# Kernel optimization log

Hardware: AMD Instinct MI355X
Metric: run time of the kernel (lower is better)

## Reference

```python
import jax, jax.numpy as jnp
import numpy as np


def setup_inputs() -> dict:
    key = jax.random.key(0)
    ks = jax.random.split(key, 5)
    B, S, F = 32, 2048, 64
    s = lambda d: 1.0 / np.sqrt(d)
    return {
        "x": jax.random.normal(ks[0], (B, S, F), jnp.float32),
        "Wq": jax.random.normal(ks[1], (F, 24), jnp.float32) * s(F),
        "Wk": jax.random.normal(ks[2], (F, 24), jnp.float32) * s(F),
        "Wv": jax.random.normal(ks[3], (F, 32), jnp.float32) * s(F),
        "Wh": jax.random.normal(ks[4], (32, F), jnp.float32) * s(32),
    }


def reference(x, Wq, Wk, Wv, Wh):
    # x: [B, S, F]
    q = jnp.einsum("bsf,fd->bsd", x, Wq)  # [B, S, 24]
    k = jnp.einsum("bsf,fd->bsd", x, Wk)  # [B, S, 24]
    v = jnp.einsum("bsf,fd->bsd", x, Wv)  # [B, S, 32]
    a = jnp.einsum("bqd,bkd->bqk", q, k)  # [B, S, S]
    # NOTE: softmax over dim=1 (query axis), as in the original module
    a = jax.nn.softmax(a, axis=1)
    h1 = jnp.einsum("bqk,bkd->bqd", a, v)  # [B, S, 32]
    return jnp.einsum("bsd,df->bsf", h1, Wh)  # [B, S, F]
```

## Files before the change

kernel.cpp:

```cpp
#include <hip/hip_runtime.h>
#include <hip/hip_fp16.h>

#define SS 2048
#define L2E 1.44269504088896340736f

typedef _Float16 f16x4 __attribute__((ext_vector_type(4)));
typedef _Float16 f16x8 __attribute__((ext_vector_type(8)));
typedef float f32x4 __attribute__((ext_vector_type(4)));

#define GLDS16(g, l) __builtin_amdgcn_global_load_lds(                          \
    (const __attribute__((address_space(1))) void*)(g),                         \
    (__attribute__((address_space(3))) void*)(l), 16, 0, 0)
#define GLDS4(g, l) __builtin_amdgcn_global_load_lds(                           \
    (const __attribute__((address_space(1))) void*)(g),                         \
    (__attribute__((address_space(3))) void*)(l), 4, 0, 0)

__global__ __launch_bounds__(256) void qkv_kernel(
    const float* __restrict__ x, const float* __restrict__ Wq,
    const float* __restrict__ Wk, const float* __restrict__ Wv,
    _Float16* __restrict__ qfp, _Float16* __restrict__ kfp,
    _Float16* __restrict__ vfp)
{
    __shared__ float xsT[64 * 64];
    __shared__ float wc[64 * 96];

    int t = threadIdx.x;
    for (int i = t; i < 384; i += 256) {
        float4 v = ((const float4*)Wq)[i];
        int f = (i * 4) / 24, c = (i * 4) % 24;
        *(float4*)&wc[f * 96 + c] = v;
    }
    for (int i = t; i < 384; i += 256) {
        float4 v = ((const float4*)Wk)[i];
        int f = (i * 4) / 24, c = (i * 4) % 24;
        *(float4*)&wc[f * 96 + 24 + c] = v;
    }
    for (int i = t; i < 512; i += 256) {
        float4 v = ((const float4*)Wv)[i];
        int f = i >> 3, c = (i * 4) & 31;
        *(float4*)&wc[f * 96 + 48 + c] = v;
    }
    {
        int f = t >> 2, seg = t & 3;
        *(float4*)&wc[f * 96 + 80 + seg * 4] = (float4){0.f, 0.f, 0.f, 0.f};
    }
    long rowbase = (long)blockIdx.x * 64;
    const float4* xg = (const float4*)(x + rowbase * 64);
    for (int i = t; i < 1024; i += 256) {
        int r = i >> 4, c4 = i & 15;
        float4 v = xg[i];
        xsT[(c4 * 4 + 0) * 64 + r] = v.x;
        xsT[(c4 * 4 + 1) * 64 + r] = v.y;
        xsT[(c4 * 4 + 2) * 64 + r] = v.z;
        xsT[(c4 * 4 + 3) * 64 + r] = v.w;
    }
    __syncthreads();

    int rg = t >> 3;
    int cg = t & 7;
    float acc0[12], acc1[12];
    #pragma unroll
    for (int i = 0; i < 12; ++i) acc0[i] = acc1[i] = 0.f;

    #pragma unroll 4
    for (int f = 0; f < 64; ++f) {
        float2 xv = *(const float2*)&xsT[f * 64 + rg * 2];
        const float* wr = &wc[f * 96 + cg * 12];
        float4 wA = *(const float4*)(wr);
        float4 wB = *(const float4*)(wr + 4);
        float4 wC = *(const float4*)(wr + 8);
        float wv_[12] = {wA.x, wA.y, wA.z, wA.w, wB.x, wB.y, wB.z, wB.w,
                         wC.x, wC.y, wC.z, wC.w};
        #pragma unroll
        for (int i = 0; i < 12; ++i) {
            acc0[i] += xv.x * wv_[i];
            acc1[i] += xv.y * wv_[i];
        }
    }
    __syncthreads();
    _Float16* os = (_Float16*)wc;

    if (t < 128) {
        int reg = t >> 6, rr = t & 63;
        *(f16x8*)&os[reg * 2048 + (rr >> 4) * 512 + (48 + (rr & 15)) * 8]
            = (f16x8){0, 0, 0, 0, 0, 0, 0, 0};
    }

    #pragma unroll
    for (int j = 0; j < 2; ++j) {
        int s = rg * 2 + j, st = s >> 4;
        const float* a = j ? acc1 : acc0;
        #pragma unroll
        for (int i = 0; i < 12; ++i) {
            int c = cg * 12 + i;
            if (c < 24) {
                os[st * 512 + ((c >> 3) * 16 + (s & 15)) * 8 + (c & 7)]
                    = (_Float16)(a[i] * L2E);
            } else if (c < 48) {
                int ck = c - 24;
                os[2048 + st * 512 + ((ck >> 3) * 16 + (s & 15)) * 8 + (ck & 7)]
                    = (_Float16)a[i];
            } else if (c < 80) {
                int vd = c - 48;
                os[4096 + st * 512 + (((s >> 2) & 3) * 16 + (vd & 15)) * 8
                   + (vd >> 4) * 4 + (s & 3)] = (_Float16)a[i];
            }
        }
    }
    __syncthreads();

    long blk = blockIdx.x;
    *(f16x8*)(qfp + blk * 2048 + t * 8) = *(const f16x8*)&os[t * 8];
    *(f16x8*)(kfp + blk * 2048 + t * 8) = *(const f16x8*)&os[2048 + t * 8];
    *(f16x8*)(vfp + blk * 2048 + t * 8) = *(const f16x8*)&os[4096 + t * 8];
}

__global__ __launch_bounds__(256) void stats_kernel(
    const _Float16* __restrict__ qf, const _Float16* __restrict__ kf,
    float* __restrict__ zpart)
{
    __shared__ __align__(16) _Float16 qtile[2][2048];
    int w = blockIdx.x;
    int b = w >> 6, rest = w & 63;
    int kb = rest >> 3, qs = rest & 7;
    int t = threadIdx.x;
    int wv = t >> 6, l = t & 63, llo = l & 15, lhi = l >> 4;

    const _Float16* kfb = kf + ((long)b * 128 + kb * 16 + wv * 4) * 512 + l * 8;
    f16x8 af[4];
    #pragma unroll
    for (int kt = 0; kt < 4; ++kt) af[kt] = *(const f16x8*)(kfb + kt * 512);

    const _Float16* qsrc = qf + ((long)b * 128 + qs * 16 + wv) * 512 + l * 8;
    f32x4 z[4] = {{0,0,0,0},{0,0,0,0},{0,0,0,0},{0,0,0,0}};

    GLDS16(qsrc, &qtile[0][wv * 512]);
    for (int rnd = 0; rnd < 4; ++rnd) {
        int cb = rnd & 1;
        __syncthreads();
        if (rnd < 3) GLDS16(qsrc + (rnd + 1) * 2048, &qtile[cb ^ 1][wv * 512]);
        #pragma unroll
        for (int fi = 0; fi < 4; ++fi) {
            f16x8 q0 = *(const f16x8*)&qtile[cb][fi * 512 + l * 8];
            #pragma unroll
            for (int kt = 0; kt < 4; ++kt) {
                f32x4 d = __builtin_amdgcn_mfma_f32_16x16x32_f16(af[kt], q0,
                            (f32x4){0.f, 0.f, 0.f, 0.f}, 0, 0, 0);
                #pragma unroll
                for (int r = 0; r < 4; ++r) z[kt][r] += __builtin_amdgcn_exp2f(d[r]);
            }
        }
    }
    #pragma unroll
    for (int m = 1; m < 16; m <<= 1)
        #pragma unroll
        for (int kt = 0; kt < 4; ++kt)
            #pragma unroll
            for (int r = 0; r < 4; ++r) z[kt][r] += __shfl_xor(z[kt][r], m, 64);
    if (llo == 0) {
        #pragma unroll
        for (int kt = 0; kt < 4; ++kt)
            *(f32x4*)(zpart + ((long)qs * 32 + b) * SS + kb * 256 + wv * 64
                      + kt * 16 + lhi * 4) = z[kt];
    }
}

__global__ __launch_bounds__(256) void finalize_kernel(
    const float* __restrict__ zpart, float* __restrict__ wneg)
{
    int i = blockIdx.x * 256 + threadIdx.x;
    float s = 0.f;
    #pragma unroll
    for (int qs = 0; qs < 8; ++qs) s += zpart[(long)qs * 32 * SS + i];
    wneg[i] = -__builtin_amdgcn_logf(s);
}

__global__ __launch_bounds__(256) void attn_out_kernel(
    const _Float16* __restrict__ qf, const _Float16* __restrict__ kf,
    const _Float16* __restrict__ vf, const float* __restrict__ wneg,
    const float* __restrict__ Wh, float* __restrict__ out)
{
    __shared__ __align__(16) _Float16 lds[2][4224];

    int w = blockIdx.x;
    int b = w >> 5, qblk = w & 31;
    int t = threadIdx.x;
    int wv = t >> 6, l = t & 63, llo = l & 15, lhi = l >> 4;
    int q0 = qblk * 64 + wv * 16;

    f16x8 qfr = *(const f16x8*)(qf + ((long)b * 128 + qblk * 4 + wv) * 512 + l * 8);

    f16x4 whlo[4], whhi[4];
    #pragma unroll
    for (int fb = 0; fb < 4; ++fb)
        #pragma unroll
        for (int j = 0; j < 4; ++j) {
            whlo[fb][j] = (_Float16)Wh[(4 * lhi + j) * 64 + fb * 16 + llo];
            whhi[fb][j] = (_Float16)Wh[(16 + 4 * lhi + j) * 64 + fb * 16 + llo];
        }

    const _Float16* kgb = kf + ((long)b * 128 + wv) * 512 + l * 8;
    const _Float16* vgb = vf + (long)b * 65536 + wv * 512 + l * 8;
    const float*    wgb = wneg + (long)b * SS + l;

    f32x4 acc0 = {0,0,0,0}, acc1 = {0,0,0,0};

    GLDS16(kgb, &lds[0][wv * 512]);
    GLDS16(vgb, &lds[0][2048 + wv * 512]);
    if (wv == 0) GLDS4(wgb, (float*)&lds[0][4096]);

    for (int tile = 0; tile < 32; ++tile) {
        int cb = tile & 1;
        __syncthreads();
        if (tile < 31) {
            GLDS16(kgb + (long)(tile + 1) * 2048, &lds[cb ^ 1][wv * 512]);
            GLDS16(vgb + (long)(tile + 1) * 2048, &lds[cb ^ 1][2048 + wv * 512]);
            if (wv == 0) GLDS4(wgb + (tile + 1) * 64, (float*)&lds[cb ^ 1][4096]);
        }
        const _Float16* Kb = &lds[cb][0];
        const _Float16* Vb = &lds[cb][2048];
        const float*    Wb = (const float*)&lds[cb][4096];
        #pragma unroll
        for (int t4 = 0; t4 < 4; ++t4) {
            f16x8 kfr = *(const f16x8*)(Kb + t4 * 512 + l * 8);
            float4 w4 = *(const float4*)(Wb + t4 * 16 + lhi * 4);
            f32x4 d = __builtin_amdgcn_mfma_f32_16x16x32_f16(kfr, qfr,
                        (f32x4){w4.x, w4.y, w4.z, w4.w}, 0, 0, 0);
            f16x4 pa;
            #pragma unroll
            for (int r = 0; r < 4; ++r) pa[r] = (_Float16)__builtin_amdgcn_exp2f(d[r]);
            f16x8 v01 = *(const f16x8*)(Vb + t4 * 512 + l * 8);
            f16x4 v0 = {v01[0], v01[1], v01[2], v01[3]};
            f16x4 v1 = {v01[4], v01[5], v01[6], v01[7]};
            acc0 = __builtin_amdgcn_mfma_f32_16x16x16f16(v0, pa, acc0, 0, 0, 0);
            acc1 = __builtin_amdgcn_mfma_f32_16x16x16f16(v1, pa, acc1, 0, 0, 0);
        }
    }

    f16x4 h0, h1;
    #pragma unroll
    for (int r = 0; r < 4; ++r) {
        h0[r] = (_Float16)acc0[r];
        h1[r] = (_Float16)acc1[r];
    }
    float* orow = out + ((long)b * SS + q0 + llo) * 64 + 4 * lhi;
    #pragma unroll
    for (int fb = 0; fb < 4; ++fb) {
        f32x4 o = __builtin_amdgcn_mfma_f32_16x16x16f16(whlo[fb], h0,
                    (f32x4){0.f, 0.f, 0.f, 0.f}, 0, 0, 0);
        o = __builtin_amdgcn_mfma_f32_16x16x16f16(whhi[fb], h1, o, 0, 0, 0);
        *(f32x4*)(orow + fb * 16) = o;
    }
}

extern "C" void kernel_launch(void* const* d_in, const int* in_sizes, int n_in,
                              void* d_out, int out_size, void* d_ws, size_t ws_size,
                              hipStream_t stream) {
    const float* x  = (const float*)d_in[0];
    const float* Wq = (const float*)d_in[1];
    const float* Wk = (const float*)d_in[2];
    const float* Wv = (const float*)d_in[3];
    const float* Wh = (const float*)d_in[4];
    float* out = (float*)d_out;

    char* ws = (char*)d_ws;
    _Float16* qf  = (_Float16*)(ws);
    _Float16* kf  = (_Float16*)(ws + (4l << 20));
    _Float16* vf  = (_Float16*)(ws + (8l << 20));
    float* wneg   = (float*)(ws + (12l << 20));
    float* zpart  = (float*)(ws + (12l << 20) + (256l << 10));

    qkv_kernel<<<1024, 256, 0, stream>>>(x, Wq, Wk, Wv, qf, kf, vf);
    stats_kernel<<<2048, 256, 0, stream>>>(qf, kf, zpart);
    finalize_kernel<<<256, 256, 0, stream>>>(zpart, wneg);
    attn_out_kernel<<<1024, 256, 0, stream>>>(qf, kf, vf, wneg, Wh, out);
}
```

Before: 86.25 us.

## Compute QKV projection with fp16 MFMA instead of scalar FMA

The QKV projection kernel now converts the concatenated weights to fp16 MFMA B-fragments in shared memory and loads x rows directly into fp16 A-fragments. Each wave computes a 16-row tile with 16x16x32 MFMA instructions, replacing the scalar fp32 FMA loop and the transposed x staging. The goal is to cut ALU time in the projection stage. The cost is fp16 rounding of x and the weights before accumulation, plus an extra weight re-layout pass in every block.

```diff
diff --git a/kernel.cpp b/kernel.cpp
--- a/kernel.cpp
+++ b/kernel.cpp
@@ -21,64 +21,49 @@
     _Float16* __restrict__ qfp, _Float16* __restrict__ kfp,
     _Float16* __restrict__ vfp)
 {
-    __shared__ float xsT[64 * 64];
-    __shared__ float wc[64 * 96];
+    __shared__ float wcs[64 * 96];
+    __shared__ __align__(16) _Float16 wfb[12 * 512];
 
     int t = threadIdx.x;
+    int wv = t >> 6, l = t & 63, llo = l & 15, lhi = l >> 4;
+
     for (int i = t; i < 384; i += 256) {
         float4 v = ((const float4*)Wq)[i];
         int f = (i * 4) / 24, c = (i * 4) % 24;
-        *(float4*)&wc[f * 96 + c] = v;
+        *(float4*)&wcs[f * 96 + c] = v;
     }
     for (int i = t; i < 384; i += 256) {
         float4 v = ((const float4*)Wk)[i];
         int f = (i * 4) / 24, c = (i * 4) % 24;
-        *(float4*)&wc[f * 96 + 24 + c] = v;
+        *(float4*)&wcs[f * 96 + 32 + c] = v;
     }
     for (int i = t; i < 512; i += 256) {
         float4 v = ((const float4*)Wv)[i];
         int f = i >> 3, c = (i * 4) & 31;
-        *(float4*)&wc[f * 96 + 48 + c] = v;
+        *(float4*)&wcs[f * 96 + 64 + c] = v;
     }
     {
-        int f = t >> 2, seg = t & 3;
-        *(float4*)&wc[f * 96 + 80 + seg * 4] = (float4){0.f, 0.f, 0.f, 0.f};
-    }
-    long rowbase = (long)blockIdx.x * 64;
-    const float4* xg = (const float4*)(x + rowbase * 64);
-    for (int i = t; i < 1024; i += 256) {
-        int r = i >> 4, c4 = i & 15;
-        float4 v = xg[i];
-        xsT[(c4 * 4 + 0) * 64 + r] = v.x;
-        xsT[(c4 * 4 + 1) * 64 + r] = v.y;
-        xsT[(c4 * 4 + 2) * 64 + r] = v.z;
-        xsT[(c4 * 4 + 3) * 64 + r] = v.w;
+        int f = t >> 2, which = t & 3;
+        int c = (which < 2) ? (24 + which * 4) : (56 + (which - 2) * 4);
+        *(float4*)&wcs[f * 96 + c] = (float4){0.f, 0.f, 0.f, 0.f};
     }
     __syncthreads();
 
-    int rg = t >> 3;
-    int cg = t & 7;
-    float acc0[12], acc1[12];
-    #pragma unroll
-    for (int i = 0; i < 12; ++i) acc0[i] = acc1[i] = 0.f;
-
-    #pragma unroll 4
-    for (int f = 0; f < 64; ++f) {
-        float2 xv = *(const float2*)&xsT[f * 64 + rg * 2];
-        const float* wr = &wc[f * 96 + cg * 12];
-        float4 wA = *(const float4*)(wr);
-        float4 wB = *(const float4*)(wr + 4);
-        float4 wC = *(const float4*)(wr + 8);
-        float wv_[12] = {wA.x, wA.y, wA.z, wA.w, wB.x, wB.y, wB.z, wB.w,
-                         wC.x, wC.y, wC.z, wC.w};
-        #pragma unroll
-        for (int i = 0; i < 12; ++i) {
-            acc0[i] += xv.x * wv_[i];
-            acc1[i] += xv.y * wv_[i];
-        }
+    #pragma unroll
+    for (int p = 0; p < 3; ++p) {
+        int sidx = t + p * 256;
+        int fr = sidx >> 6, lane = sidx & 63;
+        int ct = fr >> 1, kk = fr & 1;
+        int lls = lane & 15, lhs = lane >> 4;
+        f16x8 wfr;
+        #pragma unroll
+        for (int j = 0; j < 8; ++j)
+            wfr[j] = (_Float16)wcs[(kk * 32 + lhs * 8 + j) * 96 + ct * 16 + lls];
+        *(f16x8*)&wfb[fr * 512 + lane * 8] = wfr;
     }
     __syncthreads();
-    _Float16* os = (_Float16*)wc;
+
+    _Float16* os = (_Float16*)wcs;
 
     if (t < 128) {
         int reg = t >> 6, rr = t & 63;
@@ -86,26 +71,47 @@
             = (f16x8){0, 0, 0, 0, 0, 0, 0, 0};
     }
 
-    #pragma unroll
-    for (int j = 0; j < 2; ++j) {
-        int s = rg * 2 + j, st = s >> 4;
-        const float* a = j ? acc1 : acc0;
-        #pragma unroll
-        for (int i = 0; i < 12; ++i) {
-            int c = cg * 12 + i;
-            if (c < 24) {
-                os[st * 512 + ((c >> 3) * 16 + (s & 15)) * 8 + (c & 7)]
-                    = (_Float16)(a[i] * L2E);
-            } else if (c < 48) {
-                int ck = c - 24;
-                os[2048 + st * 512 + ((ck >> 3) * 16 + (s & 15)) * 8 + (ck & 7)]
-                    = (_Float16)a[i];
-            } else if (c < 80) {
-                int vd = c - 48;
-                os[4096 + st * 512 + (((s >> 2) & 3) * 16 + (vd & 15)) * 8
-                   + (vd >> 4) * 4 + (s & 3)] = (_Float16)a[i];
-            }
-        }
+    long rowbase = (long)blockIdx.x * 64;
+    const float* xr = x + (rowbase + wv * 16 + llo) * 64 + lhi * 8;
+    f16x8 a0, a1;
+    {
+        float4 u0 = *(const float4*)(xr);
+        float4 u1 = *(const float4*)(xr + 4);
+        float4 u2 = *(const float4*)(xr + 32);
+        float4 u3 = *(const float4*)(xr + 36);
+        a0[0] = (_Float16)u0.x; a0[1] = (_Float16)u0.y;
+        a0[2] = (_Float16)u0.z; a0[3] = (_Float16)u0.w;
+        a0[4] = (_Float16)u1.x; a0[5] = (_Float16)u1.y;
+        a0[6] = (_Float16)u1.z; a0[7] = (_Float16)u1.w;
+        a1[0] = (_Float16)u2.x; a1[1] = (_Float16)u2.y;
+        a1[2] = (_Float16)u2.z; a1[3] = (_Float16)u2.w;
+        a1[4] = (_Float16)u3.x; a1[5] = (_Float16)u3.y;
+        a1[6] = (_Float16)u3.z; a1[7] = (_Float16)u3.w;
+    }
+
+    f32x4 d[6];
+    #pragma unroll
+    for (int ct = 0; ct < 6; ++ct) {
+        f16x8 b0 = *(const f16x8*)&wfb[(ct * 2 + 0) * 512 + l * 8];
+        f16x8 b1 = *(const f16x8*)&wfb[(ct * 2 + 1) * 512 + l * 8];
+        d[ct] = __builtin_amdgcn_mfma_f32_16x16x32_f16(a0, b0,
+                  (f32x4){0.f, 0.f, 0.f, 0.f}, 0, 0, 0);
+        d[ct] = __builtin_amdgcn_mfma_f32_16x16x32_f16(a1, b1, d[ct], 0, 0, 0);
+    }
+
+    #pragma unroll
+    for (int r = 0; r < 4; ++r) {
+        int sl = lhi * 4 + r;
+        os[wv * 512 + ((llo >> 3) * 16 + sl) * 8 + (llo & 7)]
+            = (_Float16)(d[0][r] * L2E);
+        if (llo < 8)
+            os[wv * 512 + (32 + sl) * 8 + llo] = (_Float16)(d[1][r] * L2E);
+        os[2048 + wv * 512 + ((llo >> 3) * 16 + sl) * 8 + (llo & 7)]
+            = (_Float16)d[2][r];
+        if (llo < 8)
+            os[2048 + wv * 512 + (32 + sl) * 8 + llo] = (_Float16)d[3][r];
+        os[4096 + wv * 512 + (lhi * 16 + llo) * 8 + r]     = (_Float16)d[4][r];
+        os[4096 + wv * 512 + (lhi * 16 + llo) * 8 + 4 + r] = (_Float16)d[5][r];
     }
     __syncthreads();
 
```

After: 72.99 us. -15.4%, faster.
